# Kernel optimization log

Hardware: AMD Instinct MI355X
Metric: run time of the kernel (lower is better)

## Reference

```python
import jax, jax.numpy as jnp
import numpy as np

B, T, F = 512, 256, 128
H, FF, OUT = 512, 1024, 64
PAD = -999.0


def setup_inputs() -> dict:
    key = jax.random.key(0)
    ks = jax.random.split(key, 10)
    x = jax.random.normal(ks[0], (B, T, F), dtype=jnp.float32)
    seq_lens = jax.random.randint(ks[1], (B,), 0, T)
    seq_lens = jnp.maximum(seq_lens, 1)  # at least one valid timestep per sample
    # apply end-of-sequence padding with the padding indicator value
    t_idx = jnp.arange(T)
    pad_mask = t_idx[None, :] >= seq_lens[:, None]  # [B, T] True where padded
    x = jnp.where(pad_mask[:, :, None], PAD, x)
    s = 0.02
    W_ih = jax.random.normal(ks[2], (3 * H, F), dtype=jnp.float32) * s
    W_hh = jax.random.normal(ks[3], (3 * H, H), dtype=jnp.float32) * s
    b_ih = jax.random.normal(ks[4], (3 * H,), dtype=jnp.float32) * s
    b_hh = jax.random.normal(ks[5], (3 * H,), dtype=jnp.float32) * s
    W1 = jax.random.normal(ks[6], (H, FF), dtype=jnp.float32) * s
    b1 = jnp.zeros((FF,), dtype=jnp.float32)
    W2 = jax.random.normal(ks[7], (FF, OUT), dtype=jnp.float32) * s
    b2 = jnp.zeros((OUT,), dtype=jnp.float32)
    return {"x": x, "seq_lens": seq_lens, "W_ih": W_ih, "W_hh": W_hh,
            "b_ih": b_ih, "b_hh": b_hh, "W1": W1, "b1": b1, "W2": W2, "b2": b2}


def _run(x, seq_lens, W_ih, W_hh, b_ih, b_hh, W1, b1, W2, b2):
    valid = jnp.arange(T)[None, :] < seq_lens[:, None]  # [B, T]

    def gru_step(h, inp):
        x_t, v = inp  # x_t: [B, F], v: [B]
        gi = x_t @ W_ih.T + b_ih            # [B, 3H]
        gh = h @ W_hh.T + b_hh              # [B, 3H]
        i_r, i_z, i_n = jnp.split(gi, 3, axis=-1)
        h_r, h_z, h_n = jnp.split(gh, 3, axis=-1)
        r = jax.nn.sigmoid(i_r + h_r)
        z = jax.nn.sigmoid(i_z + h_z)
        n = jnp.tanh(i_n + r * h_n)
        h_new = (1.0 - z) * n + z * h
        # packed-sequence semantics: hidden only advances on valid steps;
        # padded output positions are filled with the padding indicator
        h = jnp.where(v[:, None], h_new, h)
        out = jnp.where(v[:, None], h_new, PAD)
        return h, out

    h0 = jnp.zeros((B, H), dtype=x.dtype)
    xs = (jnp.swapaxes(x, 0, 1), jnp.swapaxes(valid, 0, 1))  # time-major
    _, rnn_out_t = jax.lax.scan(gru_step, h0, xs)             # [T, B, H]
    rnn_out = jnp.swapaxes(rnn_out_t, 0, 1)                   # [B, T, H]

    # apply_to_each_timestep: FF head on non-padded rows only, padded rows
    # get fill value = padding_indicator
    ff_in = jnp.where(valid[:, :, None], rnn_out, 0.0)
    hid = jax.nn.relu(jnp.einsum('bth,hf->btf', ff_in, W1) + b1)
    y = jnp.einsum('btf,fo->bto', hid, W2) + b2               # [B, T, OUT]
    y = jnp.where(valid[:, :, None], y, PAD)
    return y


def reference(x, seq_lens, W_ih, W_hh, b_ih, b_hh, W1, b1, W2, b2):
    return _run(x, seq_lens, W_ih, W_hh, b_ih, b_hh, W1, b1, W2, b2)
```

## Files before the change

kernel.cpp:

```cpp
#include <hip/hip_runtime.h>

#define BB 512
#define TT 256
#define FDIM 128
#define HDIM 512
#define FFD 1024
#define OUTD 64
#define PADV -999.0f
#define NBLK 256
#define NTHR 256
#define PGRP (4 * 64 * 16)
#define PSLOT (8 * PGRP)

typedef __bf16 bf16_t;
typedef bf16_t bf16x8 __attribute__((ext_vector_type(8)));
typedef float f32x4 __attribute__((ext_vector_type(4)));
typedef unsigned int u32;
typedef u32 u32x4 __attribute__((ext_vector_type(4)));
typedef unsigned long long u64;

union LdsU {
  struct {
    u32 rzf[80 * 256];
    u32 nhf[32 * 256];
    u32 nif[8 * 256];
    float  ex[4][64][33];
    u64 hprev[64][8];
  } a;
  struct {
    u32 w1f[64 * 256];
    u32 w2f[8 * 256];
    bf16_t st[64 * 72];
  } b;
};

__device__ __forceinline__ f32x4 mfma16(bf16x8 a, bf16x8 b, f32x4 c) {
  return __builtin_amdgcn_mfma_f32_16x16x32_bf16(a, b, c, 0, 0, 0);
}
__device__ __forceinline__ float sigm(float x) { return 1.f / (1.f + __expf(-x)); }
__device__ __forceinline__ float tanh_f(float x) { return 2.f / (1.f + __expf(-2.f * x)) - 1.f; }

__device__ __forceinline__ void wait_flags(unsigned* f1, unsigned v1,
                                           unsigned* f2, unsigned v2) {
  const int l = threadIdx.x & 63;
  if (l < 32) {
    unsigned* p = (l < 16) ? (f1 + l) : (f2 + (l - 16));
    const unsigned v = (l < 16) ? v1 : v2;
    while (__hip_atomic_load(p, __ATOMIC_RELAXED, __HIP_MEMORY_SCOPE_AGENT) < v)
      __builtin_amdgcn_s_sleep(1);
  }
}


__global__ __launch_bounds__(NTHR) void gru_net_kernel(
    const float* __restrict__ x, const int* __restrict__ seq,
    const float* __restrict__ Wih, const float* __restrict__ Whh,
    const float* __restrict__ bih, const float* __restrict__ bhh,
    const float* __restrict__ W1, const float* __restrict__ b1,
    const float* __restrict__ W2, const float* __restrict__ b2,
    float* __restrict__ out,
    bf16_t* __restrict__ hb, bf16_t* __restrict__ ff, bf16_t* __restrict__ hd,
    float* __restrict__ psc, unsigned* __restrict__ bar) {
  __shared__ LdsU L;
  __shared__ float biasA[4][32];
  __shared__ float b1s[64];
  __shared__ float b2s[16];
  __shared__ int   seqA[64];
  __shared__ int   seqC[64];

  const int blk = blockIdx.x, tid = threadIdx.x;
  const int wv = tid >> 6, lane = tid & 63;
  const int q = lane >> 4, col16 = lane & 15, q8 = q * 8;
  const bool isA = blk < 128;

  const int grp = isA ? (blk & 7) : ((blk - 128) & 7);
  unsigned* flagA = bar + grp * 32;
  unsigned* flagB = bar + (8 + grp) * 32;

  int b0 = 0, c0 = 0, f0 = 0;
  if (isA) {
    const int sib = blk >> 3;
    b0 = (blk & 7) * 64;
    c0 = sib * 32;
    for (int i = tid; i < 80 * 64; i += NTHR) {
      const int ln = i & 63, fi = i >> 6;
      const int j = fi / 20, ks = fi - j * 20;
      const int cc = ln & 15, qq = ln >> 4;
      const int colj = j * 16 + cc;
      const int grow = (colj < 32) ? (c0 + colj) : (512 + c0 + (colj - 32));
      bf16_t tmp[8];
      if (ks < 4) {
        const float* src = Wih + (size_t)grow * FDIM + ks * 32 + qq * 8;
        for (int e = 0; e < 8; ++e) tmp[e] = (bf16_t)src[e];
      } else {
        const float* src = Whh + (size_t)grow * HDIM + (ks - 4) * 32 + qq * 8;
        for (int e = 0; e < 8; ++e) tmp[e] = (bf16_t)src[e];
      }
      const u32* t32 = (const u32*)tmp;
      u32* dst = &L.a.rzf[fi * 256 + ln];
      dst[0] = t32[0]; dst[64] = t32[1]; dst[128] = t32[2]; dst[192] = t32[3];
    }
    for (int i = tid; i < 32 * 64; i += NTHR) {
      const int ln = i & 63, fi = i >> 6;
      const int j2 = fi >> 4, ks = fi & 15;
      const int cc = ln & 15, qq = ln >> 4;
      const int grow = 1024 + c0 + j2 * 16 + cc;
      const float* src = Whh + (size_t)grow * HDIM + ks * 32 + qq * 8;
      bf16_t tmp[8];
      for (int e = 0; e < 8; ++e) tmp[e] = (bf16_t)src[e];
      const u32* t32 = (const u32*)tmp;
      u32* dst = &L.a.nhf[fi * 256 + ln];
      dst[0] = t32[0]; dst[64] = t32[1]; dst[128] = t32[2]; dst[192] = t32[3];
    }
    for (int i = tid; i < 8 * 64; i += NTHR) {
      const int ln = i & 63, fi = i >> 6;
      const int j2 = fi >> 2, ks = fi & 3;
      const int cc = ln & 15, qq = ln >> 4;
      const int grow = 1024 + c0 + j2 * 16 + cc;
      const float* src = Wih + (size_t)grow * FDIM + ks * 32 + qq * 8;
      bf16_t tmp[8];
      for (int e = 0; e < 8; ++e) tmp[e] = (bf16_t)src[e];
      const u32* t32 = (const u32*)tmp;
      u32* dst = &L.a.nif[fi * 256 + ln];
      dst[0] = t32[0]; dst[64] = t32[1]; dst[128] = t32[2]; dst[192] = t32[3];
    }
    if (tid < 32) {
      biasA[0][tid] = bih[c0 + tid] + bhh[c0 + tid];
      biasA[1][tid] = bih[512 + c0 + tid] + bhh[512 + c0 + tid];
      biasA[2][tid] = bih[1024 + c0 + tid];
      biasA[3][tid] = bhh[1024 + c0 + tid];
    }
    if (tid < 64) seqA[tid] = seq[b0 + tid];

    for (int i = tid; i < 512; i += NTHR) {
      const int r = i >> 3, cq = (i & 7) * 4;
      __hip_atomic_store((u64*)(hb + (size_t)BB * HDIM + (size_t)(b0 + r) * HDIM + c0 + cq),
                         0ull, __ATOMIC_RELAXED, __HIP_MEMORY_SCOPE_AGENT);
      ((u64*)L.a.hprev)[i] = 0ull;
    }
    __syncthreads();
    if (tid == 0)
      __hip_atomic_store(&flagA[sib], 1u, __ATOMIC_RELAXED, __HIP_MEMORY_SCOPE_AGENT);

    for (int t = 0; t < TT; ++t) {
      const int rA = b0 + wv * 16 + col16;
      const float* paxf = x + ((size_t)rA * TT + t) * FDIM;
      const f32x4 zz = {0.f, 0.f, 0.f, 0.f};
      f32x4 acc[4] = {zz, zz, zz, zz};
      f32x4 accn[2] = {zz, zz};
      f32x4 acci[2] = {zz, zz};
      #pragma unroll
      for (int ks = 0; ks < 4; ++ks) {
        const int ko = ks * 32 + q8;
        const float4 u0 = *(const float4*)(paxf + ko);
        const float4 u1 = *(const float4*)(paxf + ko + 4);
        bf16x8 av;
        av[0]=(bf16_t)u0.x; av[1]=(bf16_t)u0.y; av[2]=(bf16_t)u0.z; av[3]=(bf16_t)u0.w;
        av[4]=(bf16_t)u1.x; av[5]=(bf16_t)u1.y; av[6]=(bf16_t)u1.z; av[7]=(bf16_t)u1.w;
        #pragma unroll
        for (int j = 0; j < 4; ++j) {
          const u32* pz = &L.a.rzf[(size_t)(j * 20 + ks) * 256 + lane];
          const u32x4 tz = {pz[0], pz[64], pz[128], pz[192]};
          acc[j] = mfma16(av, *(const bf16x8*)&tz, acc[j]);
        }
        #pragma unroll
        for (int j = 0; j < 2; ++j) {
          const u32* pn = &L.a.nif[(size_t)(j * 4 + ks) * 256 + lane];
          const u32x4 tn = {pn[0], pn[64], pn[128], pn[192]};
          acci[j] = mfma16(av, *(const bf16x8*)&tn, acci[j]);
        }
      }
      if (wv == 0)
        wait_flags(flagA, (unsigned)(t + 1), flagB, (t >= 2) ? (unsigned)(t - 1) : 0u);
      __syncthreads();

      bf16_t* hr = hb + (size_t)((t + 1) & 1) * BB * HDIM;
      bf16_t* hw = hb + (size_t)(t & 1) * BB * HDIM;
      bf16_t* fw = ff + (size_t)(t & 1) * BB * HDIM;
      bf16_t* pah = hr + (size_t)rA * HDIM;
      #pragma unroll
      for (int kp = 0; kp < 4; ++kp) {
        const int ks0 = kp * 4, ks1 = kp * 4 + 1, ks2 = kp * 4 + 2, ks3 = kp * 4 + 3;
        const int ko0 = ks0 * 32 + q8, ko1 = ks1 * 32 + q8;
        const int ko2 = ks2 * 32 + q8, ko3 = ks3 * 32 + q8;
        u64 hqa[2];
        u64 hqb[2];
        u64 hqc[2];
        u64 hqd[2];
        hqa[0] = __hip_atomic_load((u64*)(pah + ko0),     __ATOMIC_RELAXED, __HIP_MEMORY_SCOPE_AGENT);
        hqa[1] = __hip_atomic_load((u64*)(pah + ko0) + 1, __ATOMIC_RELAXED, __HIP_MEMORY_SCOPE_AGENT);
        hqb[0] = __hip_atomic_load((u64*)(pah + ko1),     __ATOMIC_RELAXED, __HIP_MEMORY_SCOPE_AGENT);
        hqb[1] = __hip_atomic_load((u64*)(pah + ko1) + 1, __ATOMIC_RELAXED, __HIP_MEMORY_SCOPE_AGENT);
        hqc[0] = __hip_atomic_load((u64*)(pah + ko2),     __ATOMIC_RELAXED, __HIP_MEMORY_SCOPE_AGENT);
        hqc[1] = __hip_atomic_load((u64*)(pah + ko2) + 1, __ATOMIC_RELAXED, __HIP_MEMORY_SCOPE_AGENT);
        hqd[0] = __hip_atomic_load((u64*)(pah + ko3),     __ATOMIC_RELAXED, __HIP_MEMORY_SCOPE_AGENT);
        hqd[1] = __hip_atomic_load((u64*)(pah + ko3) + 1, __ATOMIC_RELAXED, __HIP_MEMORY_SCOPE_AGENT);
        const bf16x8 av0 = *(const bf16x8*)hqa;
        const bf16x8 av1 = *(const bf16x8*)hqb;
        const bf16x8 av2 = *(const bf16x8*)hqc;
        const bf16x8 av3 = *(const bf16x8*)hqd;
        #pragma unroll
        for (int j = 0; j < 4; ++j) {
          const u32* pz = &L.a.rzf[(size_t)(j * 20 + 4 + ks0) * 256 + lane];
          const u32x4 tz = {pz[0], pz[64], pz[128], pz[192]};
          acc[j] = mfma16(av0, *(const bf16x8*)&tz, acc[j]);
        }
        #pragma unroll
        for (int j = 0; j < 2; ++j) {
          const u32* pn = &L.a.nhf[(size_t)(j * 16 + ks0) * 256 + lane];
          const u32x4 tn = {pn[0], pn[64], pn[128], pn[192]};
          accn[j] = mfma16(av0, *(const bf16x8*)&tn, accn[j]);
        }
        #pragma unroll
        for (int j = 0; j < 4; ++j) {
          const u32* pz = &L.a.rzf[(size_t)(j * 20 + 4 + ks1) * 256 + lane];
          const u32x4 tz = {pz[0], pz[64], pz[128], pz[192]};
          acc[j] = mfma16(av1, *(const bf16x8*)&tz, acc[j]);
        }
        #pragma unroll
        for (int j = 0; j < 2; ++j) {
          const u32* pn = &L.a.nhf[(size_t)(j * 16 + ks1) * 256 + lane];
          const u32x4 tn = {pn[0], pn[64], pn[128], pn[192]};
          accn[j] = mfma16(av1, *(const bf16x8*)&tn, accn[j]);
        }
        #pragma unroll
        for (int j = 0; j < 4; ++j) {
          const u32* pz = &L.a.rzf[(size_t)(j * 20 + 4 + ks2) * 256 + lane];
          const u32x4 tz = {pz[0], pz[64], pz[128], pz[192]};
          acc[j] = mfma16(av2, *(const bf16x8*)&tz, acc[j]);
        }
        #pragma unroll
        for (int j = 0; j < 2; ++j) {
          const u32* pn = &L.a.nhf[(size_t)(j * 16 + ks2) * 256 + lane];
          const u32x4 tn = {pn[0], pn[64], pn[128], pn[192]};
          accn[j] = mfma16(av2, *(const bf16x8*)&tn, accn[j]);
        }
        #pragma unroll
        for (int j = 0; j < 4; ++j) {
          const u32* pz = &L.a.rzf[(size_t)(j * 20 + 4 + ks3) * 256 + lane];
          const u32x4 tz = {pz[0], pz[64], pz[128], pz[192]};
          acc[j] = mfma16(av3, *(const bf16x8*)&tz, acc[j]);
        }
        #pragma unroll
        for (int j = 0; j < 2; ++j) {
          const u32* pn = &L.a.nhf[(size_t)(j * 16 + ks3) * 256 + lane];
          const u32x4 tn = {pn[0], pn[64], pn[128], pn[192]};
          accn[j] = mfma16(av3, *(const bf16x8*)&tn, accn[j]);
        }
      }
      #pragma unroll
      for (int j = 0; j < 4; ++j) {
        const int sl = j >> 1, cb = (j & 1) * 16 + col16;
        #pragma unroll
        for (int rg = 0; rg < 4; ++rg)
          L.a.ex[sl][wv * 16 + q * 4 + rg][cb] = acc[j][rg];
      }
      #pragma unroll
      for (int j = 0; j < 2; ++j) {
        const int cb = j * 16 + col16;
        #pragma unroll
        for (int rg = 0; rg < 4; ++rg) {
          L.a.ex[2][wv * 16 + q * 4 + rg][cb] = accn[j][rg];
          L.a.ex[3][wv * 16 + q * 4 + rg][cb] = acci[j][rg];
        }
      }
      __syncthreads();
      for (int e = tid; e < 512; e += NTHR) {
        const int row = e >> 3, cq = (e & 7) << 2;
        const int bidx = b0 + row;
        const u64 hp8 = L.a.hprev[row][cq >> 2];
        const bf16_t* hp4 = (const bf16_t*)&hp8;
        bf16_t hw4[4], fw4[4];
        const bool v = (t < seqA[row]);
        #pragma unroll
        for (int j = 0; j < 4; ++j) {
          const int c = cq + j;
          const float gr  = L.a.ex[0][row][c] + biasA[0][c];
          const float gz  = L.a.ex[1][row][c] + biasA[1][c];
          const float gnh = L.a.ex[2][row][c] + biasA[3][c];
          const float gni = L.a.ex[3][row][c] + biasA[2][c];
          const float r = sigm(gr), zg = sigm(gz);
          const float n = tanh_f(gni + r * gnh);
          const float hp = (float)hp4[j];
          const float hnew = (1.f - zg) * n + zg * hp;
          hw4[j] = (bf16_t)(v ? hnew : hp);
          fw4[j] = (bf16_t)(v ? hnew : 0.f);
        }
        L.a.hprev[row][cq >> 2] = *(u64*)hw4;
        __hip_atomic_store((u64*)(hw + (size_t)bidx * HDIM + c0 + cq), *(u64*)hw4,
                           __ATOMIC_RELAXED, __HIP_MEMORY_SCOPE_AGENT);
        __hip_atomic_store((u64*)(fw + (size_t)bidx * HDIM + c0 + cq), *(u64*)fw4,
                           __ATOMIC_RELAXED, __HIP_MEMORY_SCOPE_AGENT);
      }
      __syncthreads();
      if (tid == 0)
        __hip_atomic_store(&flagA[sib], (unsigned)(t + 2), __ATOMIC_RELAXED, __HIP_MEMORY_SCOPE_AGENT);
    }
  } else {
    const int cidx = blk - 128;
    const int fc = cidx >> 3;
    const int oc = fc & 3;
    const int kq = fc >> 2;
    const bool isFin = (fc < 4);
    b0 = (cidx & 7) * 64;
    f0 = fc * 64;
    const int o0 = oc * 16;
    for (int i = tid; i < 64 * 64; i += NTHR) {
      const int ln = i & 63, fi = i >> 6;
      const int j = fi >> 4, ks = fi & 15;
      const int cc = ln & 15, qq = ln >> 4;
      const int fcol = f0 + j * 16 + cc;
      const int kb = ks * 32 + qq * 8;
      bf16_t tmp[8];
      for (int e = 0; e < 8; ++e) tmp[e] = (bf16_t)W1[(size_t)(kb + e) * FFD + fcol];
      const u32* t32 = (const u32*)tmp;
      u32* dst = &L.b.w1f[fi * 256 + ln];
      dst[0] = t32[0]; dst[64] = t32[1]; dst[128] = t32[2]; dst[192] = t32[3];
    }
    if (tid < 64) b1s[tid] = b1[f0 + tid];
    for (int i = tid; i < 8 * 64; i += NTHR) {
      const int ln = i & 63, ks = i >> 6;
      const int cc = ln & 15, qq = ln >> 4;
      const int kb = kq * 256 + ks * 32 + qq * 8;
      bf16_t tmp[8];
      for (int e = 0; e < 8; ++e) tmp[e] = (bf16_t)W2[(kb + e) * OUTD + o0 + cc];
      const u32* t32 = (const u32*)tmp;
      u32* dst = &L.b.w2f[ks * 256 + ln];
      dst[0] = t32[0]; dst[64] = t32[1]; dst[128] = t32[2]; dst[192] = t32[3];
    }
    if (isFin) {
      if (tid < 16) b2s[tid] = b2[o0 + tid];
      if (tid < 64) seqC[tid] = seq[b0 + tid];
    }
    __syncthreads();

    float* pg = psc + (size_t)grp * PGRP + (size_t)oc * (64 * 16);
    for (int u = 0; u <= TT + 1; ++u) {
      if (wv == 0)
        wait_flags(flagB, (unsigned)u, flagA, (u < TT) ? (unsigned)(u + 2) : 0u);
      __syncthreads();

      const int rCF = b0 + wv * 16 + col16;
      bf16_t* paF = hd + (size_t)((u - 1) & 1) * BB * FFD + (size_t)rCF * FFD + kq * 256 + q8;
      u64 fz0a = 0, fz0b = 0, fz1a = 0, fz1b = 0, fz2a = 0, fz2b = 0, fz3a = 0, fz3b = 0;
      u64 fz4a = 0, fz4b = 0, fz5a = 0, fz5b = 0, fz6a = 0, fz6b = 0, fz7a = 0, fz7b = 0;
      if (u >= 1 && u <= TT) {
        fz0a = __hip_atomic_load((u64*)(paF + 0 * 32),     __ATOMIC_RELAXED, __HIP_MEMORY_SCOPE_AGENT);
        fz0b = __hip_atomic_load((u64*)(paF + 0 * 32) + 1, __ATOMIC_RELAXED, __HIP_MEMORY_SCOPE_AGENT);
        fz1a = __hip_atomic_load((u64*)(paF + 1 * 32),     __ATOMIC_RELAXED, __HIP_MEMORY_SCOPE_AGENT);
        fz1b = __hip_atomic_load((u64*)(paF + 1 * 32) + 1, __ATOMIC_RELAXED, __HIP_MEMORY_SCOPE_AGENT);
        fz2a = __hip_atomic_load((u64*)(paF + 2 * 32),     __ATOMIC_RELAXED, __HIP_MEMORY_SCOPE_AGENT);
        fz2b = __hip_atomic_load((u64*)(paF + 2 * 32) + 1, __ATOMIC_RELAXED, __HIP_MEMORY_SCOPE_AGENT);
        fz3a = __hip_atomic_load((u64*)(paF + 3 * 32),     __ATOMIC_RELAXED, __HIP_MEMORY_SCOPE_AGENT);
        fz3b = __hip_atomic_load((u64*)(paF + 3 * 32) + 1, __ATOMIC_RELAXED, __HIP_MEMORY_SCOPE_AGENT);
        fz4a = __hip_atomic_load((u64*)(paF + 4 * 32),     __ATOMIC_RELAXED, __HIP_MEMORY_SCOPE_AGENT);
        fz4b = __hip_atomic_load((u64*)(paF + 4 * 32) + 1, __ATOMIC_RELAXED, __HIP_MEMORY_SCOPE_AGENT);
        fz5a = __hip_atomic_load((u64*)(paF + 5 * 32),     __ATOMIC_RELAXED, __HIP_MEMORY_SCOPE_AGENT);
        fz5b = __hip_atomic_load((u64*)(paF + 5 * 32) + 1, __ATOMIC_RELAXED, __HIP_MEMORY_SCOPE_AGENT);
        fz6a = __hip_atomic_load((u64*)(paF + 6 * 32),     __ATOMIC_RELAXED, __HIP_MEMORY_SCOPE_AGENT);
        fz6b = __hip_atomic_load((u64*)(paF + 6 * 32) + 1, __ATOMIC_RELAXED, __HIP_MEMORY_SCOPE_AGENT);
        fz7a = __hip_atomic_load((u64*)(paF + 7 * 32),     __ATOMIC_RELAXED, __HIP_MEMORY_SCOPE_AGENT);
        fz7b = __hip_atomic_load((u64*)(paF + 7 * 32) + 1, __ATOMIC_RELAXED, __HIP_MEMORY_SCOPE_AGENT);
      }
      float* ppF = pg + (size_t)((u - 2) & 1) * PSLOT + (tid >> 2) * 16 + (tid & 3) * 4;
      u64 fp0 = 0, fp1 = 0;
      if (isFin && u >= 2) {
        fp0 = __hip_atomic_load((u64*)ppF,     __ATOMIC_RELAXED, __HIP_MEMORY_SCOPE_AGENT);
        fp1 = __hip_atomic_load((u64*)ppF + 1, __ATOMIC_RELAXED, __HIP_MEMORY_SCOPE_AGENT);
      }

      if (u < TT) {
        const int t = u;
        bf16_t* fr = ff + (size_t)(t & 1) * BB * HDIM;
        bf16_t* hwid = hd + (size_t)(t & 1) * BB * FFD;
        const int rB = b0 + wv * 16 + col16;
        bf16_t* pa = fr + (size_t)rB * HDIM;
        const f32x4 zz = {0.f, 0.f, 0.f, 0.f};
        f32x4 acc[4] = {zz, zz, zz, zz};
        #pragma unroll
        for (int kp = 0; kp < 4; ++kp) {
          const int ks0 = kp * 4, ks1 = kp * 4 + 1, ks2 = kp * 4 + 2, ks3 = kp * 4 + 3;
          const int ko0 = ks0 * 32 + q8, ko1 = ks1 * 32 + q8;
          const int ko2 = ks2 * 32 + q8, ko3 = ks3 * 32 + q8;
          u64 fqa[2];
          u64 fqb[2];
          u64 fqc[2];
          u64 fqd[2];
          fqa[0] = __hip_atomic_load((u64*)(pa + ko0),     __ATOMIC_RELAXED, __HIP_MEMORY_SCOPE_AGENT);
          fqa[1] = __hip_atomic_load((u64*)(pa + ko0) + 1, __ATOMIC_RELAXED, __HIP_MEMORY_SCOPE_AGENT);
          fqb[0] = __hip_atomic_load((u64*)(pa + ko1),     __ATOMIC_RELAXED, __HIP_MEMORY_SCOPE_AGENT);
          fqb[1] = __hip_atomic_load((u64*)(pa + ko1) + 1, __ATOMIC_RELAXED, __HIP_MEMORY_SCOPE_AGENT);
          fqc[0] = __hip_atomic_load((u64*)(pa + ko2),     __ATOMIC_RELAXED, __HIP_MEMORY_SCOPE_AGENT);
          fqc[1] = __hip_atomic_load((u64*)(pa + ko2) + 1, __ATOMIC_RELAXED, __HIP_MEMORY_SCOPE_AGENT);
          fqd[0] = __hip_atomic_load((u64*)(pa + ko3),     __ATOMIC_RELAXED, __HIP_MEMORY_SCOPE_AGENT);
          fqd[1] = __hip_atomic_load((u64*)(pa + ko3) + 1, __ATOMIC_RELAXED, __HIP_MEMORY_SCOPE_AGENT);
          const bf16x8 av0 = *(const bf16x8*)fqa;
          const bf16x8 av1 = *(const bf16x8*)fqb;
          const bf16x8 av2 = *(const bf16x8*)fqc;
          const bf16x8 av3 = *(const bf16x8*)fqd;
          #pragma unroll
          for (int j = 0; j < 4; ++j) {
            const u32* pw = &L.b.w1f[(size_t)(j * 16 + ks0) * 256 + lane];
            const u32x4 tw = {pw[0], pw[64], pw[128], pw[192]};
            acc[j] = mfma16(av0, *(const bf16x8*)&tw, acc[j]);
          }
          #pragma unroll
          for (int j = 0; j < 4; ++j) {
            const u32* pw = &L.b.w1f[(size_t)(j * 16 + ks1) * 256 + lane];
            const u32x4 tw = {pw[0], pw[64], pw[128], pw[192]};
            acc[j] = mfma16(av1, *(const bf16x8*)&tw, acc[j]);
          }
          #pragma unroll
          for (int j = 0; j < 4; ++j) {
            const u32* pw = &L.b.w1f[(size_t)(j * 16 + ks2) * 256 + lane];
            const u32x4 tw = {pw[0], pw[64], pw[128], pw[192]};
            acc[j] = mfma16(av2, *(const bf16x8*)&tw, acc[j]);
          }
          #pragma unroll
          for (int j = 0; j < 4; ++j) {
            const u32* pw = &L.b.w1f[(size_t)(j * 16 + ks3) * 256 + lane];
            const u32x4 tw = {pw[0], pw[64], pw[128], pw[192]};
            acc[j] = mfma16(av3, *(const bf16x8*)&tw, acc[j]);
          }
        }
        #pragma unroll
        for (int j = 0; j < 4; ++j) {
          const int fcc = j * 16 + col16;
          #pragma unroll
          for (int rg = 0; rg < 4; ++rg)
            L.b.st[(wv * 16 + q * 4 + rg) * 72 + fcc] =
                (bf16_t)fmaxf(acc[j][rg] + b1s[fcc], 0.f);
        }
        __syncthreads();
        for (int w = tid; w < 1024; w += NTHR) {
          const int r = w >> 4, cq = (w & 15) * 4;
          const u64 pk = *(const u64*)&L.b.st[r * 72 + cq];
          __hip_atomic_store((u64*)(hwid + (size_t)(b0 + r) * FFD + f0 + cq), pk,
                             __ATOMIC_RELAXED, __HIP_MEMORY_SCOPE_AGENT);
        }
      }
      if (u >= 1 && u <= TT) {
        const int t = u - 1;
        f32x4 acc = {0.f, 0.f, 0.f, 0.f};
        {
          u64 w0[2] = {fz0a, fz0b};
          const u32* pw = &L.b.w2f[(size_t)0 * 256 + lane];
          const u32x4 tw = {pw[0], pw[64], pw[128], pw[192]};
          acc = mfma16(*(const bf16x8*)w0, *(const bf16x8*)&tw, acc);
        }
        {
          u64 w1v[2] = {fz1a, fz1b};
          const u32* pw = &L.b.w2f[(size_t)1 * 256 + lane];
          const u32x4 tw = {pw[0], pw[64], pw[128], pw[192]};
          acc = mfma16(*(const bf16x8*)w1v, *(const bf16x8*)&tw, acc);
        }
        {
          u64 w2v[2] = {fz2a, fz2b};
          const u32* pw = &L.b.w2f[(size_t)2 * 256 + lane];
          const u32x4 tw = {pw[0], pw[64], pw[128], pw[192]};
          acc = mfma16(*(const bf16x8*)w2v, *(const bf16x8*)&tw, acc);
        }
        {
          u64 w3v[2] = {fz3a, fz3b};
          const u32* pw = &L.b.w2f[(size_t)3 * 256 + lane];
          const u32x4 tw = {pw[0], pw[64], pw[128], pw[192]};
          acc = mfma16(*(const bf16x8*)w3v, *(const bf16x8*)&tw, acc);
        }
        {
          u64 w4v[2] = {fz4a, fz4b};
          const u32* pw = &L.b.w2f[(size_t)4 * 256 + lane];
          const u32x4 tw = {pw[0], pw[64], pw[128], pw[192]};
          acc = mfma16(*(const bf16x8*)w4v, *(const bf16x8*)&tw, acc);
        }
        {
          u64 w5v[2] = {fz5a, fz5b};
          const u32* pw = &L.b.w2f[(size_t)5 * 256 + lane];
          const u32x4 tw = {pw[0], pw[64], pw[128], pw[192]};
          acc = mfma16(*(const bf16x8*)w5v, *(const bf16x8*)&tw, acc);
        }
        {
          u64 w6v[2] = {fz6a, fz6b};
          const u32* pw = &L.b.w2f[(size_t)6 * 256 + lane];
          const u32x4 tw = {pw[0], pw[64], pw[128], pw[192]};
          acc = mfma16(*(const bf16x8*)w6v, *(const bf16x8*)&tw, acc);
        }
        {
          u64 w7v[2] = {fz7a, fz7b};
          const u32* pw = &L.b.w2f[(size_t)7 * 256 + lane];
          const u32x4 tw = {pw[0], pw[64], pw[128], pw[192]};
          acc = mfma16(*(const bf16x8*)w7v, *(const bf16x8*)&tw, acc);
        }
        float* pb = pg + (size_t)(t & 1) * PSLOT;
        #pragma unroll
        for (int rg = 0; rg < 4; ++rg)
          atomicAdd(pb + (wv * 16 + q * 4 + rg) * 16 + col16, acc[rg]);
      }
      if (isFin && u >= 2) {
        const int t2 = u - 2;
        float pv[4];
        ((u64*)pv)[0] = fp0;
        ((u64*)pv)[1] = fp1;
        const int row = tid >> 2, c4 = (tid & 3) * 4;
        const bool v = (t2 < seqC[row]);
        float* po = out + ((size_t)(b0 + row) * TT + t2) * OUTD + o0 + c4;
        #pragma unroll
        for (int j = 0; j < 4; ++j)
          po[j] = v ? (pv[j] + b2s[c4 + j]) : PADV;
        __hip_atomic_store((u64*)ppF,     0ull, __ATOMIC_RELAXED, __HIP_MEMORY_SCOPE_AGENT);
        __hip_atomic_store((u64*)ppF + 1, 0ull, __ATOMIC_RELAXED, __HIP_MEMORY_SCOPE_AGENT);
      }
      __syncthreads();
      if (tid == 0)
        __hip_atomic_store(&flagB[fc], (unsigned)(u + 1), __ATOMIC_RELAXED, __HIP_MEMORY_SCOPE_AGENT);
    }
  }
}

extern "C" void kernel_launch(void* const* d_in, const int* in_sizes, int n_in,
                              void* d_out, int out_size, void* d_ws, size_t ws_size,
                              hipStream_t stream) {
  const float* x   = (const float*)d_in[0];
  const int*   seq = (const int*)d_in[1];
  const float* Wih = (const float*)d_in[2];
  const float* Whh = (const float*)d_in[3];
  const float* bih = (const float*)d_in[4];
  const float* bhh = (const float*)d_in[5];
  const float* W1  = (const float*)d_in[6];
  const float* b1  = (const float*)d_in[7];
  const float* W2  = (const float*)d_in[8];
  const float* b2  = (const float*)d_in[9];
  float* out = (float*)d_out;
  char* ws = (char*)d_ws;

  unsigned* bar = (unsigned*)ws;
  float* psc = (float*)(ws + 4096);
  bf16_t* hb = (bf16_t*)(ws + 4096 + 2 * PSLOT * 4);
  bf16_t* ff = hb + (size_t)2 * BB * HDIM;
  bf16_t* hd = ff + (size_t)2 * BB * HDIM;

  hipMemsetAsync(ws, 0, 4096 + 2 * PSLOT * 4, stream);
  void* args[] = {&x, &seq, &Wih, &Whh, &bih, &bhh, &W1, &b1, &W2, &b2,
                  &out, &hb, &ff, &hd, &psc, &bar};
  hipLaunchCooperativeKernel((void*)gru_net_kernel, dim3(NBLK), dim3(NTHR),
                             args, 0, stream);
}
```

Baseline: 2.228 ms.

## Double threads per block and split MFMA output tiles across wave halves

Raises the block size from 256 to 512 threads. Each pair of waves now shares one 16-row slice, with each wave computing half of the gate/FF output column tiles and half of the W2 K-range. This is meant to cut the serial per-wave MFMA chain inside each latency-bound recurrent timestep. The cost is more waves per block, more atomicAdd traffic to the partial sums (two waves now add into each element), and more register and occupancy pressure.

```diff
diff --git a/kernel.cpp b/kernel.cpp
--- a/kernel.cpp
+++ b/kernel.cpp
@@ -8,7 +8,7 @@
 #define OUTD 64
 #define PADV -999.0f
 #define NBLK 256
-#define NTHR 256
+#define NTHR 512
 #define PGRP (4 * 64 * 16)
 #define PSLOT (8 * PGRP)
 
@@ -70,6 +70,7 @@
 
   const int blk = blockIdx.x, tid = threadIdx.x;
   const int wv = tid >> 6, lane = tid & 63;
+  const int wrow = wv & 3, whalf = wv >> 2;
   const int q = lane >> 4, col16 = lane & 15, q8 = q * 8;
   const bool isA = blk < 128;
 
@@ -142,13 +143,15 @@
     if (tid == 0)
       __hip_atomic_store(&flagA[sib], 1u, __ATOMIC_RELAXED, __HIP_MEMORY_SCOPE_AGENT);
 
+    const int j0 = whalf * 2, j1 = whalf * 2 + 1, jn = whalf;
+
     for (int t = 0; t < TT; ++t) {
-      const int rA = b0 + wv * 16 + col16;
+      const int rA = b0 + wrow * 16 + col16;
       const float* paxf = x + ((size_t)rA * TT + t) * FDIM;
       const f32x4 zz = {0.f, 0.f, 0.f, 0.f};
-      f32x4 acc[4] = {zz, zz, zz, zz};
-      f32x4 accn[2] = {zz, zz};
-      f32x4 acci[2] = {zz, zz};
+      f32x4 acc0 = zz, acc1 = zz;
+      f32x4 accn = zz;
+      f32x4 acci = zz;
       #pragma unroll
       for (int ks = 0; ks < 4; ++ks) {
         const int ko = ks * 32 + q8;
@@ -157,17 +160,20 @@
         bf16x8 av;
         av[0]=(bf16_t)u0.x; av[1]=(bf16_t)u0.y; av[2]=(bf16_t)u0.z; av[3]=(bf16_t)u0.w;
         av[4]=(bf16_t)u1.x; av[5]=(bf16_t)u1.y; av[6]=(bf16_t)u1.z; av[7]=(bf16_t)u1.w;
-        #pragma unroll
-        for (int j = 0; j < 4; ++j) {
-          const u32* pz = &L.a.rzf[(size_t)(j * 20 + ks) * 256 + lane];
-          const u32x4 tz = {pz[0], pz[64], pz[128], pz[192]};
-          acc[j] = mfma16(av, *(const bf16x8*)&tz, acc[j]);
-        }
-        #pragma unroll
-        for (int j = 0; j < 2; ++j) {
-          const u32* pn = &L.a.nif[(size_t)(j * 4 + ks) * 256 + lane];
+        {
+          const u32* pz = &L.a.rzf[(size_t)(j0 * 20 + ks) * 256 + lane];
+          const u32x4 tz = {pz[0], pz[64], pz[128], pz[192]};
+          acc0 = mfma16(av, *(const bf16x8*)&tz, acc0);
+        }
+        {
+          const u32* pz = &L.a.rzf[(size_t)(j1 * 20 + ks) * 256 + lane];
+          const u32x4 tz = {pz[0], pz[64], pz[128], pz[192]};
+          acc1 = mfma16(av, *(const bf16x8*)&tz, acc1);
+        }
+        {
+          const u32* pn = &L.a.nif[(size_t)(jn * 4 + ks) * 256 + lane];
           const u32x4 tn = {pn[0], pn[64], pn[128], pn[192]};
-          acci[j] = mfma16(av, *(const bf16x8*)&tn, acci[j]);
+          acci = mfma16(av, *(const bf16x8*)&tn, acci);
         }
       }
       if (wv == 0)
@@ -199,69 +205,75 @@
         const bf16x8 av1 = *(const bf16x8*)hqb;
         const bf16x8 av2 = *(const bf16x8*)hqc;
         const bf16x8 av3 = *(const bf16x8*)hqd;
-        #pragma unroll
-        for (int j = 0; j < 4; ++j) {
-          const u32* pz = &L.a.rzf[(size_t)(j * 20 + 4 + ks0) * 256 + lane];
-          const u32x4 tz = {pz[0], pz[64], pz[128], pz[192]};
-          acc[j] = mfma16(av0, *(const bf16x8*)&tz, acc[j]);
-        }
-        #pragma unroll
-        for (int j = 0; j < 2; ++j) {
-          const u32* pn = &L.a.nhf[(size_t)(j * 16 + ks0) * 256 + lane];
+        {
+          const u32* pz = &L.a.rzf[(size_t)(j0 * 20 + 4 + ks0) * 256 + lane];
+          const u32x4 tz = {pz[0], pz[64], pz[128], pz[192]};
+          acc0 = mfma16(av0, *(const bf16x8*)&tz, acc0);
+        }
+        {
+          const u32* pz = &L.a.rzf[(size_t)(j1 * 20 + 4 + ks0) * 256 + lane];
+          const u32x4 tz = {pz[0], pz[64], pz[128], pz[192]};
+          acc1 = mfma16(av0, *(const bf16x8*)&tz, acc1);
+        }
+        {
+          const u32* pn = &L.a.nhf[(size_t)(jn * 16 + ks0) * 256 + lane];
           const u32x4 tn = {pn[0], pn[64], pn[128], pn[192]};
-          accn[j] = mfma16(av0, *(const bf16x8*)&tn, accn[j]);
-        }
-        #pragma unroll
-        for (int j = 0; j < 4; ++j) {
-          const u32* pz = &L.a.rzf[(size_t)(j * 20 + 4 + ks1) * 256 + lane];
-          const u32x4 tz = {pz[0], pz[64], pz[128], pz[192]};
-          acc[j] = mfma16(av1, *(const bf16x8*)&tz, acc[j]);
-        }
-        #pragma unroll
-        for (int j = 0; j < 2; ++j) {
-          const u32* pn = &L.a.nhf[(size_t)(j * 16 + ks1) * 256 + lane];
+          accn = mfma16(av0, *(const bf16x8*)&tn, accn);
+        }
+        {
+          const u32* pz = &L.a.rzf[(size_t)(j0 * 20 + 4 + ks1) * 256 + lane];
+          const u32x4 tz = {pz[0], pz[64], pz[128], pz[192]};
+          acc0 = mfma16(av1, *(const bf16x8*)&tz, acc0);
+        }
+        {
+          const u32* pz = &L.a.rzf[(size_t)(j1 * 20 + 4 + ks1) * 256 + lane];
+          const u32x4 tz = {pz[0], pz[64], pz[128], pz[192]};
+          acc1 = mfma16(av1, *(const bf16x8*)&tz, acc1);
+        }
+        {
+          const u32* pn = &L.a.nhf[(size_t)(jn * 16 + ks1) * 256 + lane];
           const u32x4 tn = {pn[0], pn[64], pn[128], pn[192]};
-          accn[j] = mfma16(av1, *(const bf16x8*)&tn, accn[j]);
-        }
-        #pragma unroll
-        for (int j = 0; j < 4; ++j) {
-          const u32* pz = &L.a.rzf[(size_t)(j * 20 + 4 + ks2) * 256 + lane];
-          const u32x4 tz = {pz[0], pz[64], pz[128], pz[192]};
-          acc[j] = mfma16(av2, *(const bf16x8*)&tz, acc[j]);
-        }
-        #pragma unroll
-        for (int j = 0; j < 2; ++j) {
-          const u32* pn = &L.a.nhf[(size_t)(j * 16 + ks2) * 256 + lane];
+          accn = mfma16(av1, *(const bf16x8*)&tn, accn);
+        }
+        {
+          const u32* pz = &L.a.rzf[(size_t)(j0 * 20 + 4 + ks2) * 256 + lane];
+          const u32x4 tz = {pz[0], pz[64], pz[128], pz[192]};
+          acc0 = mfma16(av2, *(const bf16x8*)&tz, acc0);
+        }
+        {
+          const u32* pz = &L.a.rzf[(size_t)(j1 * 20 + 4 + ks2) * 256 + lane];
+          const u32x4 tz = {pz[0], pz[64], pz[128], pz[192]};
+          acc1 = mfma16(av2, *(const bf16x8*)&tz, acc1);
+        }
+        {
+          const u32* pn = &L.a.nhf[(size_t)(jn * 16 + ks2) * 256 + lane];
           const u32x4 tn = {pn[0], pn[64], pn[128], pn[192]};
-          accn[j] = mfma16(av2, *(const bf16x8*)&tn, accn[j]);
-        }
-        #pragma unroll
-        for (int j = 0; j < 4; ++j) {
-          const u32* pz = &L.a.rzf[(size_t)(j * 20 + 4 + ks3) * 256 + lane];
-          const u32x4 tz = {pz[0], pz[64], pz[128], pz[192]};
-          acc[j] = mfma16(av3, *(const bf16x8*)&tz, acc[j]);
-        }
-        #pragma unroll
-        for (int j = 0; j < 2; ++j) {
-          const u32* pn = &L.a.nhf[(size_t)(j * 16 + ks3) * 256 + lane];
+          accn = mfma16(av2, *(const bf16x8*)&tn, accn);
+        }
+        {
+          const u32* pz = &L.a.rzf[(size_t)(j0 * 20 + 4 + ks3) * 256 + lane];
+          const u32x4 tz = {pz[0], pz[64], pz[128], pz[192]};
+          acc0 = mfma16(av3, *(const bf16x8*)&tz, acc0);
+        }
+        {
+          const u32* pz = &L.a.rzf[(size_t)(j1 * 20 + 4 + ks3) * 256 + lane];
+          const u32x4 tz = {pz[0], pz[64], pz[128], pz[192]};
+          acc1 = mfma16(av3, *(const bf16x8*)&tz, acc1);
+        }
+        {
+          const u32* pn = &L.a.nhf[(size_t)(jn * 16 + ks3) * 256 + lane];
           const u32x4 tn = {pn[0], pn[64], pn[128], pn[192]};
-          accn[j] = mfma16(av3, *(const bf16x8*)&tn, accn[j]);
-        }
-      }
-      #pragma unroll
-      for (int j = 0; j < 4; ++j) {
-        const int sl = j >> 1, cb = (j & 1) * 16 + col16;
-        #pragma unroll
-        for (int rg = 0; rg < 4; ++rg)
-          L.a.ex[sl][wv * 16 + q * 4 + rg][cb] = acc[j][rg];
-      }
-      #pragma unroll
-      for (int j = 0; j < 2; ++j) {
-        const int cb = j * 16 + col16;
+          accn = mfma16(av3, *(const bf16x8*)&tn, accn);
+        }
+      }
+      {
+        const int rb = wrow * 16 + q * 4;
         #pragma unroll
         for (int rg = 0; rg < 4; ++rg) {
-          L.a.ex[2][wv * 16 + q * 4 + rg][cb] = accn[j][rg];
-          L.a.ex[3][wv * 16 + q * 4 + rg][cb] = acci[j][rg];
+          L.a.ex[whalf][rb + rg][col16]      = acc0[rg];
+          L.a.ex[whalf][rb + rg][16 + col16] = acc1[rg];
+          L.a.ex[2][rb + rg][jn * 16 + col16] = accn[rg];
+          L.a.ex[3][rb + rg][jn * 16 + col16] = acci[rg];
         }
       }
       __syncthreads();
@@ -334,16 +346,19 @@
     }
     __syncthreads();
 
+    const int j0 = whalf * 2, j1 = whalf * 2 + 1;
+
     float* pg = psc + (size_t)grp * PGRP + (size_t)oc * (64 * 16);
     for (int u = 0; u <= TT + 1; ++u) {
       if (wv == 0)
         wait_flags(flagB, (unsigned)u, flagA, (u < TT) ? (unsigned)(u + 2) : 0u);
       __syncthreads();
 
-      const int rCF = b0 + wv * 16 + col16;
-      bf16_t* paF = hd + (size_t)((u - 1) & 1) * BB * FFD + (size_t)rCF * FFD + kq * 256 + q8;
-      u64 fz0a = 0, fz0b = 0, fz1a = 0, fz1b = 0, fz2a = 0, fz2b = 0, fz3a = 0, fz3b = 0;
-      u64 fz4a = 0, fz4b = 0, fz5a = 0, fz5b = 0, fz6a = 0, fz6b = 0, fz7a = 0, fz7b = 0;
+      const int rCF = b0 + wrow * 16 + col16;
+      bf16_t* paF = hd + (size_t)((u - 1) & 1) * BB * FFD + (size_t)rCF * FFD
+                    + kq * 256 + whalf * 128 + q8;
+      u64 fz0a = 0, fz0b = 0, fz1a = 0, fz1b = 0;
+      u64 fz2a = 0, fz2b = 0, fz3a = 0, fz3b = 0;
       if (u >= 1 && u <= TT) {
         fz0a = __hip_atomic_load((u64*)(paF + 0 * 32),     __ATOMIC_RELAXED, __HIP_MEMORY_SCOPE_AGENT);
         fz0b = __hip_atomic_load((u64*)(paF + 0 * 32) + 1, __ATOMIC_RELAXED, __HIP_MEMORY_SCOPE_AGENT);
@@ -353,18 +368,10 @@
         fz2b = __hip_atomic_load((u64*)(paF + 2 * 32) + 1, __ATOMIC_RELAXED, __HIP_MEMORY_SCOPE_AGENT);
         fz3a = __hip_atomic_load((u64*)(paF + 3 * 32),     __ATOMIC_RELAXED, __HIP_MEMORY_SCOPE_AGENT);
         fz3b = __hip_atomic_load((u64*)(paF + 3 * 32) + 1, __ATOMIC_RELAXED, __HIP_MEMORY_SCOPE_AGENT);
-        fz4a = __hip_atomic_load((u64*)(paF + 4 * 32),     __ATOMIC_RELAXED, __HIP_MEMORY_SCOPE_AGENT);
-        fz4b = __hip_atomic_load((u64*)(paF + 4 * 32) + 1, __ATOMIC_RELAXED, __HIP_MEMORY_SCOPE_AGENT);
-        fz5a = __hip_atomic_load((u64*)(paF + 5 * 32),     __ATOMIC_RELAXED, __HIP_MEMORY_SCOPE_AGENT);
-        fz5b = __hip_atomic_load((u64*)(paF + 5 * 32) + 1, __ATOMIC_RELAXED, __HIP_MEMORY_SCOPE_AGENT);
-        fz6a = __hip_atomic_load((u64*)(paF + 6 * 32),     __ATOMIC_RELAXED, __HIP_MEMORY_SCOPE_AGENT);
-        fz6b = __hip_atomic_load((u64*)(paF + 6 * 32) + 1, __ATOMIC_RELAXED, __HIP_MEMORY_SCOPE_AGENT);
-        fz7a = __hip_atomic_load((u64*)(paF + 7 * 32),     __ATOMIC_RELAXED, __HIP_MEMORY_SCOPE_AGENT);
-        fz7b = __hip_atomic_load((u64*)(paF + 7 * 32) + 1, __ATOMIC_RELAXED, __HIP_MEMORY_SCOPE_AGENT);
       }
       float* ppF = pg + (size_t)((u - 2) & 1) * PSLOT + (tid >> 2) * 16 + (tid & 3) * 4;
       u64 fp0 = 0, fp1 = 0;
-      if (isFin && u >= 2) {
+      if (isFin && u >= 2 && tid < 256) {
         fp0 = __hip_atomic_load((u64*)ppF,     __ATOMIC_RELAXED, __HIP_MEMORY_SCOPE_AGENT);
         fp1 = __hip_atomic_load((u64*)ppF + 1, __ATOMIC_RELAXED, __HIP_MEMORY_SCOPE_AGENT);
       }
@@ -373,10 +380,10 @@
         const int t = u;
         bf16_t* fr = ff + (size_t)(t & 1) * BB * HDIM;
         bf16_t* hwid = hd + (size_t)(t & 1) * BB * FFD;
-        const int rB = b0 + wv * 16 + col16;
+        const int rB = b0 + wrow * 16 + col16;
         bf16_t* pa = fr + (size_t)rB * HDIM;
         const f32x4 zz = {0.f, 0.f, 0.f, 0.f};
-        f32x4 acc[4] = {zz, zz, zz, zz};
+        f32x4 acc0 = zz, acc1 = zz;
         #pragma unroll
         for (int kp = 0; kp < 4; ++kp) {
           const int ks0 = kp * 4, ks1 = kp * 4 + 1, ks2 = kp * 4 + 2, ks3 = kp * 4 + 3;
@@ -398,38 +405,55 @@
           const bf16x8 av1 = *(const bf16x8*)fqb;
           const bf16x8 av2 = *(const bf16x8*)fqc;
           const bf16x8 av3 = *(const bf16x8*)fqd;
+          {
+            const u32* pw = &L.b.w1f[(size_t)(j0 * 16 + ks0) * 256 + lane];
+            const u32x4 tw = {pw[0], pw[64], pw[128], pw[192]};
+            acc0 = mfma16(av0, *(const bf16x8*)&tw, acc0);
+          }
+          {
+            const u32* pw = &L.b.w1f[(size_t)(j1 * 16 + ks0) * 256 + lane];
+            const u32x4 tw = {pw[0], pw[64], pw[128], pw[192]};
+            acc1 = mfma16(av0, *(const bf16x8*)&tw, acc1);
+          }
+          {
+            const u32* pw = &L.b.w1f[(size_t)(j0 * 16 + ks1) * 256 + lane];
+            const u32x4 tw = {pw[0], pw[64], pw[128], pw[192]};
+            acc0 = mfma16(av1, *(const bf16x8*)&tw, acc0);
+          }
+          {
+            const u32* pw = &L.b.w1f[(size_t)(j1 * 16 + ks1) * 256 + lane];
+            const u32x4 tw = {pw[0], pw[64], pw[128], pw[192]};
+            acc1 = mfma16(av1, *(const bf16x8*)&tw, acc1);
+          }
+          {
+            const u32* pw = &L.b.w1f[(size_t)(j0 * 16 + ks2) * 256 + lane];
+            const u32x4 tw = {pw[0], pw[64], pw[128], pw[192]};
+            acc0 = mfma16(av2, *(const bf16x8*)&tw, acc0);
+          }
+          {
+            const u32* pw = &L.b.w1f[(size_t)(j1 * 16 + ks2) * 256 + lane];
+            const u32x4 tw = {pw[0], pw[64], pw[128], pw[192]};
+            acc1 = mfma16(av2, *(const bf16x8*)&tw, acc1);
+          }
+          {
+            const u32* pw = &L.b.w1f[(size_t)(j0 * 16 + ks3) * 256 + lane];
+            const u32x4 tw = {pw[0], pw[64], pw[128], pw[192]};
+            acc0 = mfma16(av3, *(const bf16x8*)&tw, acc0);
+          }
+          {
+            const u32* pw = &L.b.w1f[(size_t)(j1 * 16 + ks3) * 256 + lane];
+            const u32x4 tw = {pw[0], pw[64], pw[128], pw[192]};
+            acc1 = mfma16(av3, *(const bf16x8*)&tw, acc1);
+          }
+        }
+        {
+          const int rb = wrow * 16 + q * 4;
           #pragma unroll
-          for (int j = 0; j < 4; ++j) {
-            const u32* pw = &L.b.w1f[(size_t)(j * 16 + ks0) * 256 + lane];
-            const u32x4 tw = {pw[0], pw[64], pw[128], pw[192]};
-            acc[j] = mfma16(av0, *(const bf16x8*)&tw, acc[j]);
-          }
-          #pragma unroll
-          for (int j = 0; j < 4; ++j) {
-            const u32* pw = &L.b.w1f[(size_t)(j * 16 + ks1) * 256 + lane];
-            const u32x4 tw = {pw[0], pw[64], pw[128], pw[192]};
-            acc[j] = mfma16(av1, *(const bf16x8*)&tw, acc[j]);
-          }
-          #pragma unroll
-          for (int j = 0; j < 4; ++j) {
-            const u32* pw = &L.b.w1f[(size_t)(j * 16 + ks2) * 256 + lane];
-            const u32x4 tw = {pw[0], pw[64], pw[128], pw[192]};
-            acc[j] = mfma16(av2, *(const bf16x8*)&tw, acc[j]);
-          }
-          #pragma unroll
-          for (int j = 0; j < 4; ++j) {
-            const u32* pw = &L.b.w1f[(size_t)(j * 16 + ks3) * 256 + lane];
-            const u32x4 tw = {pw[0], pw[64], pw[128], pw[192]};
-            acc[j] = mfma16(av3, *(const bf16x8*)&tw, acc[j]);
-          }
-        }
-        #pragma unroll
-        for (int j = 0; j < 4; ++j) {
-          const int fcc = j * 16 + col16;
-          #pragma unroll
-          for (int rg = 0; rg < 4; ++rg)
-            L.b.st[(wv * 16 + q * 4 + rg) * 72 + fcc] =
-                (bf16_t)fmaxf(acc[j][rg] + b1s[fcc], 0.f);
+          for (int rg = 0; rg < 4; ++rg) {
+            const int f0c = j0 * 16 + col16, f1c = j1 * 16 + col16;
+            L.b.st[(rb + rg) * 72 + f0c] = (bf16_t)fmaxf(acc0[rg] + b1s[f0c], 0.f);
+            L.b.st[(rb + rg) * 72 + f1c] = (bf16_t)fmaxf(acc1[rg] + b1s[f1c], 0.f);
+          }
         }
         __syncthreads();
         for (int w = tid; w < 1024; w += NTHR) {
@@ -442,60 +466,37 @@
       if (u >= 1 && u <= TT) {
         const int t = u - 1;
         f32x4 acc = {0.f, 0.f, 0.f, 0.f};
+        const int kbase = whalf * 4;
         {
           u64 w0[2] = {fz0a, fz0b};
-          const u32* pw = &L.b.w2f[(size_t)0 * 256 + lane];
+          const u32* pw = &L.b.w2f[(size_t)(kbase + 0) * 256 + lane];
           const u32x4 tw = {pw[0], pw[64], pw[128], pw[192]};
           acc = mfma16(*(const bf16x8*)w0, *(const bf16x8*)&tw, acc);
         }
         {
           u64 w1v[2] = {fz1a, fz1b};
-          const u32* pw = &L.b.w2f[(size_t)1 * 256 + lane];
+          const u32* pw = &L.b.w2f[(size_t)(kbase + 1) * 256 + lane];
           const u32x4 tw = {pw[0], pw[64], pw[128], pw[192]};
           acc = mfma16(*(const bf16x8*)w1v, *(const bf16x8*)&tw, acc);
         }
         {
           u64 w2v[2] = {fz2a, fz2b};
-          const u32* pw = &L.b.w2f[(size_t)2 * 256 + lane];
+          const u32* pw = &L.b.w2f[(size_t)(kbase + 2) * 256 + lane];
           const u32x4 tw = {pw[0], pw[64], pw[128], pw[192]};
           acc = mfma16(*(const bf16x8*)w2v, *(const bf16x8*)&tw, acc);
         }
         {
           u64 w3v[2] = {fz3a, fz3b};
-          const u32* pw = &L.b.w2f[(size_t)3 * 256 + lane];
+          const u32* pw = &L.b.w2f[(size_t)(kbase + 3) * 256 + lane];
           const u32x4 tw = {pw[0], pw[64], pw[128], pw[192]};
           acc = mfma16(*(const bf16x8*)w3v, *(const bf16x8*)&tw, acc);
-        }
-        {
-          u64 w4v[2] = {fz4a, fz4b};
-          const u32* pw = &L.b.w2f[(size_t)4 * 256 + lane];
-          const u32x4 tw = {pw[0], pw[64], pw[128], pw[192]};
-          acc = mfma16(*(const bf16x8*)w4v, *(const bf16x8*)&tw, acc);
-        }
-        {
-          u64 w5v[2] = {fz5a, fz5b};
-          const u32* pw = &L.b.w2f[(size_t)5 * 256 + lane];
-          const u32x4 tw = {pw[0], pw[64], pw[128], pw[192]};
-          acc = mfma16(*(const bf16x8*)w5v, *(const bf16x8*)&tw, acc);
-        }
-        {
-          u64 w6v[2] = {fz6a, fz6b};
-          const u32* pw = &L.b.w2f[(size_t)6 * 256 + lane];
-          const u32x4 tw = {pw[0], pw[64], pw[128], pw[192]};
-          acc = mfma16(*(const bf16x8*)w6v, *(const bf16x8*)&tw, acc);
-        }
-        {
-          u64 w7v[2] = {fz7a, fz7b};
-          const u32* pw = &L.b.w2f[(size_t)7 * 256 + lane];
-          const u32x4 tw = {pw[0], pw[64], pw[128], pw[192]};
-          acc = mfma16(*(const bf16x8*)w7v, *(const bf16x8*)&tw, acc);
         }
         float* pb = pg + (size_t)(t & 1) * PSLOT;
         #pragma unroll
         for (int rg = 0; rg < 4; ++rg)
-          atomicAdd(pb + (wv * 16 + q * 4 + rg) * 16 + col16, acc[rg]);
-      }
-      if (isFin && u >= 2) {
+          atomicAdd(pb + (wrow * 16 + q * 4 + rg) * 16 + col16, acc[rg]);
+      }
+      if (isFin && u >= 2 && tid < 256) {
         const int t2 = u - 2;
         float pv[4];
         ((u64*)pv)[0] = fp0;
```

Result: slower. 3.243 ms (+45.5%).
